# Kernel optimization log

Hardware: AMD Instinct MI355X
Metric: run time of the kernel (lower is better)

Reference implementation:

```python
import jax, jax.numpy as jnp
import numpy as np

H = 8
DK = 32
D_MODEL = H * DK


def _leaky(x):
    # LeakyReLU(negative_slope=0.1)
    return jnp.where(x > 0, x, 0.1 * x)


def _edge_feat(p_edge, W1, b1, W2, b2):
    # p_edge: [b, d_edge, n, n] -> [b, h, d_k, n, n]
    e = jnp.transpose(p_edge, (0, 2, 3, 1))          # [b, n, n, d_edge]
    e = _leaky(e @ W1 + b1) @ W2 + b2                # [b, n, n, d_model]
    b, n = e.shape[0], e.shape[1]
    e = e.reshape(b, n, n, H, DK)
    return jnp.transpose(e, (0, 3, 4, 1, 2))          # [b, h, d_k, n, n]


def setup_inputs() -> dict:
    key = jax.random.key(0)
    ks = jax.random.split(key, 24)
    b, n, d_model, d_edge, d_hidden = 2, 512, 256, 40, 32
    s = 0.05
    return {
        "query": jax.random.normal(ks[0], (b, n, d_model), jnp.float32),
        "key_": jax.random.normal(ks[1], (b, n, d_model), jnp.float32),
        "value": jax.random.normal(ks[2], (b, n, d_model), jnp.float32),
        "edges_att": jax.random.normal(ks[3], (b, d_edge, n, n), jnp.float32),
        "mask": jax.random.randint(ks[4], (b, n), 0, 2, jnp.int32),
        "Wq": jax.random.normal(ks[5], (d_model, d_model), jnp.float32) * s,
        "bq": jax.random.normal(ks[6], (d_model,), jnp.float32) * s,
        "Wk": jax.random.normal(ks[7], (d_model, d_model), jnp.float32) * s,
        "bk": jax.random.normal(ks[8], (d_model,), jnp.float32) * s,
        "Wv": jax.random.normal(ks[9], (d_model, d_model), jnp.float32) * s,
        "bv": jax.random.normal(ks[10], (d_model,), jnp.float32) * s,
        "Wo": jax.random.normal(ks[11], (d_model, d_model), jnp.float32) * s,
        "bo": jax.random.normal(ks[12], (d_model,), jnp.float32) * s,
        "rkW1": jax.random.normal(ks[13], (d_edge, d_hidden), jnp.float32) * s,
        "rkb1": jax.random.normal(ks[14], (d_hidden,), jnp.float32) * s,
        "rkW2": jax.random.normal(ks[15], (d_hidden, d_model), jnp.float32) * s,
        "rkb2": jax.random.normal(ks[16], (d_model,), jnp.float32) * s,
        "rvW1": jax.random.normal(ks[17], (d_edge, d_hidden), jnp.float32) * s,
        "rvb1": jax.random.normal(ks[18], (d_hidden,), jnp.float32) * s,
        "rvW2": jax.random.normal(ks[19], (d_hidden, d_model), jnp.float32) * s,
        "rvb2": jax.random.normal(ks[20], (d_model,), jnp.float32) * s,
        "u": jax.random.normal(ks[21], (H, DK), jnp.float32) * s,
        "v": jax.random.normal(ks[22], (H, DK), jnp.float32) * s,
    }


def reference(query, key_, value, edges_att, mask,
              Wq, bq, Wk, bk, Wv, bv, Wo, bo,
              rkW1, rkb1, rkW2, rkb2, rvW1, rvb1, rvW2, rvb2, u, v):
    b, n, _ = query.shape

    def proj(x, W, bb):
        return jnp.transpose((x @ W + bb).reshape(b, n, H, DK), (0, 2, 1, 3))  # [b,h,n,d_k]

    q = proj(query, Wq, bq)
    k = proj(key_, Wk, bk)
    val = proj(value, Wv, bv)

    relK = _edge_feat(edges_att, rkW1, rkb1, rkW2, rkb2)  # [b,h,d_k,n,n]
    relV = _edge_feat(edges_att, rvW1, rvb1, rvW2, rvb2)  # [b,h,d_k,n,n]

    inv = 1.0 / jnp.sqrt(jnp.asarray(DK, q.dtype))
    s1 = jnp.einsum('bhid,bhjd->bhij', q, k) * inv
    s2 = jnp.einsum('bhid,bhdij->bhij', q + k, relK) * inv
    s3 = jnp.einsum('bhid,hd->bhi', k, u)[..., None]      # broadcast over j
    s4 = jnp.einsum('bhdij,hd->bhij', relK, v)
    scores = s1 + s2 + s3 + s4
    scores = jnp.where(mask[:, None, None, :] == 0, jnp.asarray(-1e12, scores.dtype), scores)
    p = jax.nn.softmax(scores, axis=-1)                    # [b,h,n,n]

    o = jnp.einsum('bhij,bhjd->bhid', p, val) + jnp.einsum('bhij,bhdij->bhid', p, relV)
    x = jnp.transpose(o, (0, 2, 1, 3)).reshape(b, n, D_MODEL)
    return x @ Wo + bo
```

## Files before the change

kernel.cpp:

```cpp
#include <hip/hip_runtime.h>
#include <hip/hip_bf16.h>

#define HH 8
#define DKK 32
#define DM 256
#define NN 512
#define DE 40
#define DHID 32
#define CH 128

typedef __attribute__((ext_vector_type(4))) short short4v;
typedef __attribute__((ext_vector_type(8))) short short8v;
typedef __attribute__((ext_vector_type(4))) float f32x4;

__device__ __forceinline__ unsigned short f2bf(float x) {
    union { __hip_bfloat16 h; unsigned short u; } c;
    c.h = __float2bfloat16(x);
    return c.u;
}
__device__ __forceinline__ float bf2f(unsigned short u) {
    return __uint_as_float(((unsigned int)u) << 16);
}
__device__ __forceinline__ float bf_lo(unsigned int u){ return __uint_as_float(u << 16); }
__device__ __forceinline__ float bf_hi(unsigned int u){ return __uint_as_float(u & 0xffff0000u); }
__device__ __forceinline__ unsigned int pack2bf(float a, float b) {
    return (unsigned int)f2bf(a) | ((unsigned int)f2bf(b) << 16);
}
__device__ __forceinline__ short8v ld8(const unsigned short* p) {
    short4v lo = *(const short4v*)p;
    short4v hi = *(const short4v*)(p + 4);
    short8v r;
    r[0]=lo[0]; r[1]=lo[1]; r[2]=lo[2]; r[3]=lo[3];
    r[4]=hi[0]; r[5]=hi[1]; r[6]=hi[2]; r[7]=hi[3];
    return r;
}

__global__ __launch_bounds__(256) void proj_kernel(
    const float* __restrict__ query, const float* __restrict__ key_,
    const float* __restrict__ value,
    const float* __restrict__ Wq, const float* __restrict__ bq,
    const float* __restrict__ Wk, const float* __restrict__ bk,
    const float* __restrict__ Wv, const float* __restrict__ bv,
    float* __restrict__ Q, float* __restrict__ K, float* __restrict__ V,
    int grpPerMat)
{
    const int m  = blockIdx.x / grpPerMat;
    const int r0 = (blockIdx.x % grpPerMat) * 4;
    const float* x; const float* W; const float* bb; float* dst;
    if (m == 0)      { x = query; W = Wq; bb = bq; dst = Q; }
    else if (m == 1) { x = key_;  W = Wk; bb = bk; dst = K; }
    else             { x = value; W = Wv; bb = bv; dst = V; }
    const int c = threadIdx.x;
    const float b0 = bb[c];
    float a0 = b0, a1 = b0, a2 = b0, a3 = b0;
    for (int k = 0; k < DM; ++k) {
        const float w = W[k*DM + c];
        a0 = fmaf(x[(size_t)(r0+0)*DM + k], w, a0);
        a1 = fmaf(x[(size_t)(r0+1)*DM + k], w, a1);
        a2 = fmaf(x[(size_t)(r0+2)*DM + k], w, a2);
        a3 = fmaf(x[(size_t)(r0+3)*DM + k], w, a3);
    }
    dst[(size_t)(r0+0)*DM + c] = a0;
    dst[(size_t)(r0+1)*DM + c] = a1;
    dst[(size_t)(r0+2)*DM + c] = a2;
    dst[(size_t)(r0+3)*DM + c] = a3;
}

__global__ __launch_bounds__(256) void s1_kernel(
    const float* __restrict__ Q, const float* __restrict__ K,
    unsigned short* __restrict__ s1)
{
    const int tid = threadIdx.x;
    const int bh = blockIdx.y, b = bh >> 3, hh = bh & 7;
    const int ti = (blockIdx.x >> 3) * 64, tj = (blockIdx.x & 7) * 64;
    __shared__ float Qt[64][33];
    __shared__ float Kt[64][33];
    const int c = tid & 31, r0 = tid >> 5;
#pragma unroll
    for (int s = 0; s < 8; ++s) {
        Qt[r0 + 8*s][c] = Q[(size_t)(b*NN + ti + r0 + 8*s)*DM + hh*DKK + c];
        Kt[r0 + 8*s][c] = K[(size_t)(b*NN + tj + r0 + 8*s)*DM + hh*DKK + c];
    }
    __syncthreads();
    const int tx = tid & 15, ty = tid >> 4;
    float acc[4][4] = {};
#pragma unroll
    for (int k = 0; k < DKK; ++k) {
        float qv[4], kv[4];
#pragma unroll
        for (int u = 0; u < 4; ++u) { qv[u] = Qt[ty*4+u][k]; kv[u] = Kt[tx*4+u][k]; }
#pragma unroll
        for (int ri = 0; ri < 4; ++ri)
#pragma unroll
            for (int cj = 0; cj < 4; ++cj)
                acc[ri][cj] = fmaf(qv[ri], kv[cj], acc[ri][cj]);
    }
    const float inv = 0.17677669529663687f;
#pragma unroll
    for (int ri = 0; ri < 4; ++ri) {
        ushort4 o;
        o.x = f2bf(acc[ri][0]*inv); o.y = f2bf(acc[ri][1]*inv);
        o.z = f2bf(acc[ri][2]*inv); o.w = f2bf(acc[ri][3]*inv);
        *(ushort4*)(s1 + ((size_t)(b*HH + hh)*NN + ti + ty*4 + ri)*NN + tj + tx*4) = o;
    }
}

__global__ __launch_bounds__(256, 4) void chunk_kernel(
    const float* __restrict__ edges, const int* __restrict__ mask,
    const float* __restrict__ rkW1, const float* __restrict__ rkb1,
    const float* __restrict__ rkW2, const float* __restrict__ rkb2,
    const float* __restrict__ rvW1, const float* __restrict__ rvb1,
    const float* __restrict__ vvec,
    const float* __restrict__ Q, const float* __restrict__ K, const float* __restrict__ V,
    const unsigned short* __restrict__ s1u,
    float* __restrict__ ws_m, float* __restrict__ ws_z,
    float* __restrict__ ws_A, float* __restrict__ ws_O)
{
    const int bid = blockIdx.x;
    const int bi = bid >> 2, cq = bid & 3;
    const int b  = bi >> 9;
    const int i  = bi & 511;
    const int j0 = cq*CH;
    const int tid = threadIdx.x;
    const int h = tid >> 5, l32 = tid & 31;
    const int wid = tid >> 6, lane = tid & 63;
    const int g = lane >> 4, q16 = lane & 15;
    const int team = tid >> 6, qq = tid & 63, hq = qq >> 3;
    const int jj = tid & 127, half = tid >> 7;
    const float inv = 0.17677669529663687f;

    __shared__ __align__(16) unsigned char uni[17408];
    __shared__ __align__(16) unsigned short W1bf[64*68];
    __shared__ __align__(16) float sc[HH*132];
    __shared__ __align__(16) float gKs[HH*DKK];
    __shared__ float c0Ks[HH];

    unsigned short* E   = (unsigned short*)uni;
    unsigned short* hvT = (unsigned short*)uni;
    unsigned short* hk  = (unsigned short*)(uni + 8448);
    unsigned short* pb  = (unsigned short*)(uni + 8448);
    float* wf    = (float*)uni;
    float* paccA = (float*)uni;
    float* po    = (float*)(uni + 4096);

    const size_t ebase = (size_t)b*DE*NN*NN + (size_t)i*NN;
    const float* qrow = Q + (size_t)bi*DM;

    float ev[20];
    {
        const float* ep = edges + ebase + j0 + jj;
#pragma unroll
        for (int u = 0; u < 20; ++u) ev[u] = ep[(size_t)(half*20+u)*NN*NN];
    }

    wf[tid] = inv*(qrow[tid] + K[(size_t)bi*DM + tid]) + vvec[tid];
    {
        const int n = tid >> 2, qd = tid & 3;
#pragma unroll
        for (int kk = 0; kk < 17; ++kk) {
            const int k = qd*17 + kk;
            float v = 0.f;
            if (k < DE) v = (n < 32) ? rkW1[k*DHID + n] : rvW1[k*DHID + (n-32)];
            W1bf[n*68 + k] = f2bf(v);
        }
    }
    float biasv[4];
#pragma unroll
    for (int nt = 0; nt < 4; ++nt) {
        const int n = nt*16 + q16;
        biasv[nt] = (n < 32) ? rkb1[n] : rvb1[n-32];
    }
    __syncthreads();

    {
        float acc = 0.f;
#pragma unroll
        for (int d4 = 0; d4 < DKK/4; ++d4) {
            const float4 w4 = *(const float4*)(rkW2 + (size_t)l32*DM + h*DKK + d4*4);
            const float4 f4 = *(const float4*)(&wf[h*DKK + d4*4]);
            acc = fmaf(w4.x, f4.x, acc); acc = fmaf(w4.y, f4.y, acc);
            acc = fmaf(w4.z, f4.z, acc); acc = fmaf(w4.w, f4.w, acc);
        }
        gKs[h*DKK + l32] = acc;
        if (tid < HH) {
            float a2 = 0.f;
#pragma unroll
            for (int d = 0; d < DKK; ++d)
                a2 = fmaf(rkb2[tid*DKK + d], wf[tid*DKK + d], a2);
            c0Ks[tid] = a2;
        }
    }
    __syncthreads();

    const float* vb = V + (size_t)b*NN*DM;
    const unsigned short* s1b = s1u + (size_t)b*HH*NN*NN + (size_t)i*NN;

    {
        unsigned int* Ed = (unsigned int*)&E[jj*68 + half*20];
#pragma unroll
        for (int u = 0; u < 10; ++u) Ed[u] = pack2bf(ev[2*u], ev[2*u+1]);
        if (half) {
            unsigned int* Ez = (unsigned int*)&E[jj*68 + 40];
#pragma unroll
            for (int z = 0; z < 12; ++z) Ez[z] = 0u;
        }
    }
    __syncthreads();

    f32x4 acc[2][4];
#pragma unroll
    for (int jt = 0; jt < 2; ++jt) {
        const int jn = wid*32 + jt*16 + q16;
        short8v a0 = ld8(&E[jn*68 + g*8]);
        short8v a1 = ld8(&E[jn*68 + 32 + g*8]);
#pragma unroll
        for (int nt = 0; nt < 4; ++nt) {
            const unsigned short* wp = &W1bf[(q16 + nt*16)*68 + g*8];
            f32x4 c;
            c[0] = biasv[nt]; c[1] = biasv[nt]; c[2] = biasv[nt]; c[3] = biasv[nt];
            c = __builtin_amdgcn_mfma_f32_16x16x32_bf16(a0, ld8(wp), c, 0, 0, 0);
            c = __builtin_amdgcn_mfma_f32_16x16x32_bf16(a1, ld8(wp + 32), c, 0, 0, 0);
            acc[jt][nt] = c;
        }
    }
    __syncthreads();

#pragma unroll
    for (int jt = 0; jt < 2; ++jt) {
        const int jw = wid*32 + jt*16 + g*4;
#pragma unroll
        for (int nt = 0; nt < 4; ++nt) {
#pragma unroll
            for (int r = 0; r < 4; ++r) {
                float x = acc[jt][nt][r];
                x = x > 0.f ? x : 0.1f*x;
                const unsigned short us = f2bf(x);
                const int n = nt*16 + q16;
                if (n < 32) hk[(jw+r)*34 + n] = us;
                else        hvT[(n-32)*132 + (jw+r)] = us;
            }
        }
    }
    __syncthreads();

    {
        unsigned int hku[16];
#pragma unroll
        for (int d = 0; d < 16; ++d) hku[d] = *(const unsigned int*)&hk[jj*34 + 2*d];
        const int mk = mask[b*NN + j0 + jj];
        float racc[4];
#pragma unroll
        for (int u = 0; u < 4; ++u) racc[u] = c0Ks[half*4 + u];
#pragma unroll
        for (int d = 0; d < 16; ++d) {
            const float lo = bf_lo(hku[d]), hi = bf_hi(hku[d]);
#pragma unroll
            for (int u = 0; u < 4; ++u) {
                const int hh = half*4 + u;
                racc[u] = fmaf(gKs[hh*DKK + 2*d],     lo, racc[u]);
                racc[u] = fmaf(gKs[hh*DKK + 2*d + 1], hi, racc[u]);
            }
        }
#pragma unroll
        for (int u = 0; u < 4; ++u) {
            const int hh = half*4 + u;
            float r = racc[u] + bf2f(s1b[(size_t)hh*NN*NN + j0 + jj]);
            if (mk == 0) r = -1e12f;
            sc[hh*132 + jj] = r;
        }
    }
    __syncthreads();

    {
        float sv[4];
        float mc = -3e38f;
#pragma unroll
        for (int k = 0; k < 4; ++k) { sv[k] = sc[h*132 + l32 + 32*k]; mc = fmaxf(mc, sv[k]); }
#pragma unroll
        for (int off = 16; off; off >>= 1) mc = fmaxf(mc, __shfl_xor(mc, off, 32));
        float zc = 0.f;
#pragma unroll
        for (int k = 0; k < 4; ++k) {
            const float e = __expf(sv[k] - mc);
            pb[h*132 + l32 + 32*k] = f2bf(e);
            zc += e;
        }
#pragma unroll
        for (int off = 16; off; off >>= 1) zc += __shfl_xor(zc, off, 32);
        if (l32 == 0) {
            ws_m[(size_t)bid*8 + h] = mc;
            ws_z[(size_t)bid*8 + h] = zc;
        }
    }
    __syncthreads();

    f32x4 accAf0 = {0.f,0.f,0.f,0.f}, accAf1 = {0.f,0.f,0.f,0.f};
    float aO0 = 0.f, aO1 = 0.f, aO2 = 0.f, aO3 = 0.f;
    {
        short8v pA = ld8(&pb[q16*132 + wid*32 + g*8]);
        short8v b0 = ld8(&hvT[q16*132 + wid*32 + g*8]);
        short8v b1 = ld8(&hvT[(16+q16)*132 + wid*32 + g*8]);
        accAf0 = __builtin_amdgcn_mfma_f32_16x16x32_bf16(pA, b0, accAf0, 0, 0, 0);
        accAf1 = __builtin_amdgcn_mfma_f32_16x16x32_bf16(pA, b1, accAf1, 0, 0, 0);

        const float* vrow = vb + (size_t)(j0 + team)*DM + qq*4;
        const unsigned short* ph = pb + hq*132 + team;
#pragma unroll 4
        for (int it = 0; it < 32; ++it) {
            const float p = bf2f(ph[4*it]);
            const float4 v4 = *(const float4*)(vrow + (size_t)it*4*DM);
            aO0 = fmaf(p, v4.x, aO0); aO1 = fmaf(p, v4.y, aO1);
            aO2 = fmaf(p, v4.z, aO2); aO3 = fmaf(p, v4.w, aO3);
        }
    }
    __syncthreads();

    if (g < 2) {
#pragma unroll
        for (int r = 0; r < 4; ++r) {
            paccA[wid*256 + (4*g+r)*32 + q16]      = accAf0[r];
            paccA[wid*256 + (4*g+r)*32 + 16 + q16] = accAf1[r];
        }
    }
    *(float4*)(po + team*256 + qq*4) = make_float4(aO0, aO1, aO2, aO3);
    __syncthreads();

    ws_A[(size_t)bid*256 + tid] = paccA[tid] + paccA[256+tid] + paccA[512+tid] + paccA[768+tid];
    ws_O[(size_t)bid*256 + tid] = po[tid] + po[256+tid] + po[512+tid] + po[768+tid];
}

__global__ __launch_bounds__(256) void combine_kernel(
    const float* __restrict__ rvW2, const float* __restrict__ rvb2,
    const float* __restrict__ Wo, const float* __restrict__ bo,
    const float* __restrict__ ws_m, const float* __restrict__ ws_z,
    const float* __restrict__ ws_A, const float* __restrict__ ws_O,
    float* __restrict__ out)
{
    const int bi0 = blockIdx.x * 2;
    const int tid = threadIdx.x;
    const int h = tid >> 5;
    __shared__ float A_l[2][DM], o_l[2][DM];
    __shared__ float wqs[2][4][HH], rzs[2][HH];

    if (tid < 16) {
        const int r = tid >> 3, hh = tid & 7;
        const int bi = bi0 + r;
        float mv[4], zv[4];
#pragma unroll
        for (int q = 0; q < 4; ++q) {
            mv[q] = ws_m[(size_t)(bi*4+q)*8 + hh];
            zv[q] = ws_z[(size_t)(bi*4+q)*8 + hh];
        }
        const float mm = fmaxf(fmaxf(mv[0], mv[1]), fmaxf(mv[2], mv[3]));
        float zt = 0.f;
#pragma unroll
        for (int q = 0; q < 4; ++q) {
            const float w = __expf(mv[q] - mm);
            wqs[r][q][hh] = w;
            zt = fmaf(zv[q], w, zt);
        }
        rzs[r][hh] = 1.f / zt;
    }
    __syncthreads();

    float o1v[2];
#pragma unroll
    for (int r = 0; r < 2; ++r) {
        const int bi = bi0 + r;
        const float rz = rzs[r][h];
        float A = 0.f, o1 = 0.f;
#pragma unroll
        for (int q = 0; q < 4; ++q) {
            const float w = wqs[r][q][h];
            A  = fmaf(w, ws_A[(size_t)(bi*4+q)*256 + tid], A);
            o1 = fmaf(w, ws_O[(size_t)(bi*4+q)*256 + tid], o1);
        }
        A_l[r][tid] = A * rz;
        o1v[r] = o1 * rz;
    }
    __syncthreads();

#pragma unroll
    for (int r = 0; r < 2; ++r) {
        float o2 = rvb2[tid];
#pragma unroll
        for (int t = 0; t < DHID; ++t)
            o2 = fmaf(A_l[r][h*DKK + t], rvW2[(size_t)t*DM + tid], o2);
        o_l[r][tid] = o1v[r] + o2;
    }
    __syncthreads();

    float acc0 = bo[tid], acc1 = acc0;
#pragma unroll 4
    for (int k = 0; k < DM; ++k) {
        const float w = Wo[(size_t)k*DM + tid];
        acc0 = fmaf(o_l[0][k], w, acc0);
        acc1 = fmaf(o_l[1][k], w, acc1);
    }
    out[(size_t)(bi0+0)*DM + tid] = acc0;
    out[(size_t)(bi0+1)*DM + tid] = acc1;
}

extern "C" void kernel_launch(void* const* d_in, const int* in_sizes, int n_in,
                              void* d_out, int out_size, void* d_ws, size_t ws_size,
                              hipStream_t stream) {
    const float* query = (const float*)d_in[0];
    const float* key_  = (const float*)d_in[1];
    const float* value = (const float*)d_in[2];
    const float* edges = (const float*)d_in[3];
    const int*   mask  = (const int*)d_in[4];
    const float* Wq = (const float*)d_in[5];
    const float* bq = (const float*)d_in[6];
    const float* Wk = (const float*)d_in[7];
    const float* bk = (const float*)d_in[8];
    const float* Wv = (const float*)d_in[9];
    const float* bv = (const float*)d_in[10];
    const float* Wo = (const float*)d_in[11];
    const float* bo = (const float*)d_in[12];
    const float* rkW1 = (const float*)d_in[13];
    const float* rkb1 = (const float*)d_in[14];
    const float* rkW2 = (const float*)d_in[15];
    const float* rkb2 = (const float*)d_in[16];
    const float* rvW1 = (const float*)d_in[17];
    const float* rvb1 = (const float*)d_in[18];
    const float* rvW2 = (const float*)d_in[19];
    const float* rvb2 = (const float*)d_in[20];
    const float* vvec = (const float*)d_in[22];

    const int rows = in_sizes[0] / DM;
    const int nchunk = rows * 4;

    float* Qw = (float*)d_ws;
    float* Kw = Qw + (size_t)rows*DM;
    float* Vw = Kw + (size_t)rows*DM;
    unsigned short* s1u = (unsigned short*)(Vw + (size_t)rows*DM);
    float* ws_m = (float*)(s1u + (size_t)2*HH*NN*NN);
    float* ws_z = ws_m + (size_t)nchunk*8;
    float* ws_A = ws_z + (size_t)nchunk*8;
    float* ws_O = ws_A + (size_t)nchunk*256;

    hipLaunchKernelGGL(proj_kernel, dim3(3*rows/4), dim3(256), 0, stream,
                       query, key_, value, Wq, bq, Wk, bk, Wv, bv, Qw, Kw, Vw, rows/4);
    hipLaunchKernelGGL(s1_kernel, dim3(64, 16), dim3(256), 0, stream,
                       Qw, Kw, s1u);
    hipLaunchKernelGGL(chunk_kernel, dim3(nchunk), dim3(256), 0, stream,
                       edges, mask, rkW1, rkb1, rkW2, rkb2, rvW1, rvb1,
                       vvec, Qw, Kw, Vw, s1u, ws_m, ws_z, ws_A, ws_O);
    hipLaunchKernelGGL(combine_kernel, dim3(rows/2), dim3(256), 0, stream,
                       rvW2, rvb2, Wo, bo, ws_m, ws_z, ws_A, ws_O, (float*)d_out);
}
```

Before: 115.6 us.

## Fuse s1 into chunk kernel via MFMA and hoist per-row precompute to pre_kernel

Drops the separate s1 kernel and its bf16 score buffer in global memory. The chunk kernel now computes q·k scores directly with MFMA from bf16 Q/K copies that the projection kernel writes. The relK score term also moves to an MFMA. Per-row gK vectors and the bf16 W1 staging move into a new pre_kernel so chunk_kernel does less setup and uses less LDS, and its occupancy hint rises to 6. The cost is an extra launch, bf16 rounding of K and Q, and wasted MFMA lanes from the masked per-head B operand.

After: 117.5 us. No clear change (+1.6%).

```diff
diff --git a/kernel.cpp b/kernel.cpp
--- a/kernel.cpp
+++ b/kernel.cpp
@@ -21,8 +21,6 @@
 __device__ __forceinline__ float bf2f(unsigned short u) {
     return __uint_as_float(((unsigned int)u) << 16);
 }
-__device__ __forceinline__ float bf_lo(unsigned int u){ return __uint_as_float(u << 16); }
-__device__ __forceinline__ float bf_hi(unsigned int u){ return __uint_as_float(u & 0xffff0000u); }
 __device__ __forceinline__ unsigned int pack2bf(float a, float b) {
     return (unsigned int)f2bf(a) | ((unsigned int)f2bf(b) << 16);
 }
@@ -42,6 +40,7 @@
     const float* __restrict__ Wk, const float* __restrict__ bk,
     const float* __restrict__ Wv, const float* __restrict__ bv,
     float* __restrict__ Q, float* __restrict__ K, float* __restrict__ V,
+    unsigned short* __restrict__ qbf, unsigned short* __restrict__ Kbf,
     int grpPerMat)
 {
     const int m  = blockIdx.x / grpPerMat;
@@ -64,55 +63,73 @@
     dst[(size_t)(r0+1)*DM + c] = a1;
     dst[(size_t)(r0+2)*DM + c] = a2;
     dst[(size_t)(r0+3)*DM + c] = a3;
-}
-
-__global__ __launch_bounds__(256) void s1_kernel(
+    if (m == 0) {
+        const float inv = 0.17677669529663687f;
+        qbf[(size_t)(r0+0)*DM + c] = f2bf(a0*inv);
+        qbf[(size_t)(r0+1)*DM + c] = f2bf(a1*inv);
+        qbf[(size_t)(r0+2)*DM + c] = f2bf(a2*inv);
+        qbf[(size_t)(r0+3)*DM + c] = f2bf(a3*inv);
+    } else if (m == 1) {
+        Kbf[(size_t)(r0+0)*DM + c] = f2bf(a0);
+        Kbf[(size_t)(r0+1)*DM + c] = f2bf(a1);
+        Kbf[(size_t)(r0+2)*DM + c] = f2bf(a2);
+        Kbf[(size_t)(r0+3)*DM + c] = f2bf(a3);
+    }
+}
+
+__global__ __launch_bounds__(256) void pre_kernel(
     const float* __restrict__ Q, const float* __restrict__ K,
-    unsigned short* __restrict__ s1)
+    const float* __restrict__ vvec,
+    const float* __restrict__ rkW2, const float* __restrict__ rkb2,
+    const float* __restrict__ rkW1, const float* __restrict__ rvW1,
+    const float* __restrict__ rkb1, const float* __restrict__ rvb1,
+    float* __restrict__ gkw, unsigned short* __restrict__ w1w,
+    float* __restrict__ biasw, int rows)
 {
+    const int bid = blockIdx.x;
     const int tid = threadIdx.x;
-    const int bh = blockIdx.y, b = bh >> 3, hh = bh & 7;
-    const int ti = (blockIdx.x >> 3) * 64, tj = (blockIdx.x & 7) * 64;
-    __shared__ float Qt[64][33];
-    __shared__ float Kt[64][33];
-    const int c = tid & 31, r0 = tid >> 5;
-#pragma unroll
-    for (int s = 0; s < 8; ++s) {
-        Qt[r0 + 8*s][c] = Q[(size_t)(b*NN + ti + r0 + 8*s)*DM + hh*DKK + c];
-        Kt[r0 + 8*s][c] = K[(size_t)(b*NN + tj + r0 + 8*s)*DM + hh*DKK + c];
-    }
-    __syncthreads();
-    const int tx = tid & 15, ty = tid >> 4;
-    float acc[4][4] = {};
-#pragma unroll
-    for (int k = 0; k < DKK; ++k) {
-        float qv[4], kv[4];
-#pragma unroll
-        for (int u = 0; u < 4; ++u) { qv[u] = Qt[ty*4+u][k]; kv[u] = Kt[tx*4+u][k]; }
-#pragma unroll
-        for (int ri = 0; ri < 4; ++ri)
-#pragma unroll
-            for (int cj = 0; cj < 4; ++cj)
-                acc[ri][cj] = fmaf(qv[ri], kv[cj], acc[ri][cj]);
-    }
-    const float inv = 0.17677669529663687f;
-#pragma unroll
-    for (int ri = 0; ri < 4; ++ri) {
-        ushort4 o;
-        o.x = f2bf(acc[ri][0]*inv); o.y = f2bf(acc[ri][1]*inv);
-        o.z = f2bf(acc[ri][2]*inv); o.w = f2bf(acc[ri][3]*inv);
-        *(ushort4*)(s1 + ((size_t)(b*HH + hh)*NN + ti + ty*4 + ri)*NN + tj + tx*4) = o;
-    }
-}
-
-__global__ __launch_bounds__(256, 4) void chunk_kernel(
+    if (bid < rows) {
+        const int bi = bid;
+        const int h = tid >> 5, l32 = tid & 31;
+        const float inv = 0.17677669529663687f;
+        __shared__ __align__(16) float wf[DM];
+        wf[tid] = inv*(Q[(size_t)bi*DM + tid] + K[(size_t)bi*DM + tid]) + vvec[tid];
+        __syncthreads();
+        float acc = 0.f;
+#pragma unroll
+        for (int d4 = 0; d4 < DKK/4; ++d4) {
+            const float4 w4 = *(const float4*)(rkW2 + (size_t)l32*DM + h*DKK + d4*4);
+            const float4 f4 = *(const float4*)(&wf[h*DKK + d4*4]);
+            acc = fmaf(w4.x, f4.x, acc); acc = fmaf(w4.y, f4.y, acc);
+            acc = fmaf(w4.z, f4.z, acc); acc = fmaf(w4.w, f4.w, acc);
+        }
+        ((unsigned short*)(gkw + (size_t)bi*264))[tid] = f2bf(acc);
+        if (tid < HH) {
+            float a2 = 0.f;
+#pragma unroll
+            for (int d = 0; d < DKK; ++d)
+                a2 = fmaf(rkb2[tid*DKK + d], wf[tid*DKK + d], a2);
+            gkw[(size_t)bi*264 + 256 + tid] = a2;
+        }
+    } else {
+        const int n = tid >> 2, qd = tid & 3;
+#pragma unroll
+        for (int kk = 0; kk < 17; ++kk) {
+            const int k = qd*17 + kk;
+            float v = 0.f;
+            if (k < DE) v = (n < 32) ? rkW1[k*DHID + n] : rvW1[k*DHID + (n-32)];
+            w1w[n*68 + k] = f2bf(v);
+        }
+        if (tid < 64) biasw[tid] = (tid < 32) ? rkb1[tid] : rvb1[tid-32];
+    }
+}
+
+__global__ __launch_bounds__(256, 6) void chunk_kernel(
     const float* __restrict__ edges, const int* __restrict__ mask,
-    const float* __restrict__ rkW1, const float* __restrict__ rkb1,
-    const float* __restrict__ rkW2, const float* __restrict__ rkb2,
-    const float* __restrict__ rvW1, const float* __restrict__ rvb1,
-    const float* __restrict__ vvec,
-    const float* __restrict__ Q, const float* __restrict__ K, const float* __restrict__ V,
-    const unsigned short* __restrict__ s1u,
+    const float* __restrict__ V,
+    const unsigned short* __restrict__ qbf, const unsigned short* __restrict__ Kbf,
+    const unsigned short* __restrict__ w1w, const float* __restrict__ biasw,
+    const float* __restrict__ gkw,
     float* __restrict__ ws_m, float* __restrict__ ws_z,
     float* __restrict__ ws_A, float* __restrict__ ws_O)
 {
@@ -127,24 +144,21 @@
     const int g = lane >> 4, q16 = lane & 15;
     const int team = tid >> 6, qq = tid & 63, hq = qq >> 3;
     const int jj = tid & 127, half = tid >> 7;
-    const float inv = 0.17677669529663687f;
-
-    __shared__ __align__(16) unsigned char uni[17408];
-    __shared__ __align__(16) unsigned short W1bf[64*68];
+
+    __shared__ __align__(16) unsigned char uni[18816];
     __shared__ __align__(16) float sc[HH*132];
-    __shared__ __align__(16) float gKs[HH*DKK];
+    __shared__ __align__(16) unsigned short gkb_l[16*32];
+    __shared__ int mask_l[CH];
     __shared__ float c0Ks[HH];
 
     unsigned short* E   = (unsigned short*)uni;
     unsigned short* hvT = (unsigned short*)uni;
     unsigned short* hk  = (unsigned short*)(uni + 8448);
     unsigned short* pb  = (unsigned short*)(uni + 8448);
-    float* wf    = (float*)uni;
     float* paccA = (float*)uni;
     float* po    = (float*)(uni + 4096);
 
     const size_t ebase = (size_t)b*DE*NN*NN + (size_t)i*NN;
-    const float* qrow = Q + (size_t)bi*DM;
 
     float ev[20];
     {
@@ -153,47 +167,19 @@
         for (int u = 0; u < 20; ++u) ev[u] = ep[(size_t)(half*20+u)*NN*NN];
     }
 
-    wf[tid] = inv*(qrow[tid] + K[(size_t)bi*DM + tid]) + vvec[tid];
-    {
-        const int n = tid >> 2, qd = tid & 3;
-#pragma unroll
-        for (int kk = 0; kk < 17; ++kk) {
-            const int k = qd*17 + kk;
-            float v = 0.f;
-            if (k < DE) v = (n < 32) ? rkW1[k*DHID + n] : rvW1[k*DHID + (n-32)];
-            W1bf[n*68 + k] = f2bf(v);
-        }
-    }
+    {
+        const unsigned int* gsrc = (const unsigned int*)(gkw + (size_t)bi*264);
+        unsigned int* gdst = (unsigned int*)gkb_l;
+        gdst[tid] = (tid < 128) ? gsrc[tid] : 0u;
+        if (tid < CH) mask_l[tid] = mask[b*NN + j0 + tid];
+        if (tid < HH) c0Ks[tid] = gkw[(size_t)bi*264 + 256 + tid];
+    }
+    short8v z8 = {0,0,0,0,0,0,0,0};
+    short8v myq = z8;
+    if (q16 < HH) myq = ld8(&qbf[(size_t)bi*DM + q16*DKK + g*8]);
     float biasv[4];
 #pragma unroll
-    for (int nt = 0; nt < 4; ++nt) {
-        const int n = nt*16 + q16;
-        biasv[nt] = (n < 32) ? rkb1[n] : rvb1[n-32];
-    }
-    __syncthreads();
-
-    {
-        float acc = 0.f;
-#pragma unroll
-        for (int d4 = 0; d4 < DKK/4; ++d4) {
-            const float4 w4 = *(const float4*)(rkW2 + (size_t)l32*DM + h*DKK + d4*4);
-            const float4 f4 = *(const float4*)(&wf[h*DKK + d4*4]);
-            acc = fmaf(w4.x, f4.x, acc); acc = fmaf(w4.y, f4.y, acc);
-            acc = fmaf(w4.z, f4.z, acc); acc = fmaf(w4.w, f4.w, acc);
-        }
-        gKs[h*DKK + l32] = acc;
-        if (tid < HH) {
-            float a2 = 0.f;
-#pragma unroll
-            for (int d = 0; d < DKK; ++d)
-                a2 = fmaf(rkb2[tid*DKK + d], wf[tid*DKK + d], a2);
-            c0Ks[tid] = a2;
-        }
-    }
-    __syncthreads();
-
-    const float* vb = V + (size_t)b*NN*DM;
-    const unsigned short* s1b = s1u + (size_t)b*HH*NN*NN + (size_t)i*NN;
+    for (int nt = 0; nt < 4; ++nt) biasv[nt] = biasw[nt*16 + q16];
 
     {
         unsigned int* Ed = (unsigned int*)&E[jj*68 + half*20];
@@ -215,7 +201,7 @@
         short8v a1 = ld8(&E[jn*68 + 32 + g*8]);
 #pragma unroll
         for (int nt = 0; nt < 4; ++nt) {
-            const unsigned short* wp = &W1bf[(q16 + nt*16)*68 + g*8];
+            const unsigned short* wp = w1w + (q16 + nt*16)*68 + g*8;
             f32x4 c;
             c[0] = biasv[nt]; c[1] = biasv[nt]; c[2] = biasv[nt]; c[3] = biasv[nt];
             c = __builtin_amdgcn_mfma_f32_16x16x32_bf16(a0, ld8(wp), c, 0, 0, 0);
@@ -236,7 +222,7 @@
                 x = x > 0.f ? x : 0.1f*x;
                 const unsigned short us = f2bf(x);
                 const int n = nt*16 + q16;
-                if (n < 32) hk[(jw+r)*34 + n] = us;
+                if (n < 32) hk[(jw+r)*40 + n] = us;
                 else        hvT[(n-32)*132 + (jw+r)] = us;
             }
         }
@@ -244,29 +230,31 @@
     __syncthreads();
 
     {
-        unsigned int hku[16];
-#pragma unroll
-        for (int d = 0; d < 16; ++d) hku[d] = *(const unsigned int*)&hk[jj*34 + 2*d];
-        const int mk = mask[b*NN + j0 + jj];
-        float racc[4];
-#pragma unroll
-        for (int u = 0; u < 4; ++u) racc[u] = c0Ks[half*4 + u];
-#pragma unroll
-        for (int d = 0; d < 16; ++d) {
-            const float lo = bf_lo(hku[d]), hi = bf_hi(hku[d]);
-#pragma unroll
-            for (int u = 0; u < 4; ++u) {
-                const int hh = half*4 + u;
-                racc[u] = fmaf(gKs[hh*DKK + 2*d],     lo, racc[u]);
-                racc[u] = fmaf(gKs[hh*DKK + 2*d + 1], hi, racc[u]);
+        const unsigned short* kbase = Kbf + ((size_t)(b*NN + j0))*DM;
+        short8v gkB = ld8(&gkb_l[q16*DKK + g*8]);
+#pragma unroll
+        for (int jt = 0; jt < 2; ++jt) {
+            const int jrow = wid*32 + jt*16 + q16;
+            const float ci = (q16 < HH) ? c0Ks[q16 & 7] : 0.f;
+            f32x4 s;
+            s[0] = ci; s[1] = ci; s[2] = ci; s[3] = ci;
+#pragma unroll
+            for (int hh = 0; hh < HH; ++hh) {
+                short8v aK = ld8(&kbase[(size_t)jrow*DM + hh*DKK + g*8]);
+                short8v bq = (q16 == hh) ? myq : z8;
+                s = __builtin_amdgcn_mfma_f32_16x16x32_bf16(aK, bq, s, 0, 0, 0);
             }
-        }
-#pragma unroll
-        for (int u = 0; u < 4; ++u) {
-            const int hh = half*4 + u;
-            float r = racc[u] + bf2f(s1b[(size_t)hh*NN*NN + j0 + jj]);
-            if (mk == 0) r = -1e12f;
-            sc[hh*132 + jj] = r;
+            short8v aH = ld8(&hk[jrow*40 + g*8]);
+            s = __builtin_amdgcn_mfma_f32_16x16x32_bf16(aH, gkB, s, 0, 0, 0);
+            if (q16 < HH) {
+#pragma unroll
+                for (int r = 0; r < 4; ++r) {
+                    const int jl = wid*32 + jt*16 + g*4 + r;
+                    float v = s[r];
+                    if (mask_l[jl] == 0) v = -1e12f;
+                    sc[q16*132 + jl] = v;
+                }
+            }
         }
     }
     __syncthreads();
@@ -294,16 +282,17 @@
     }
     __syncthreads();
 
-    f32x4 accAf0 = {0.f,0.f,0.f,0.f}, accAf1 = {0.f,0.f,0.f,0.f};
-    float aO0 = 0.f, aO1 = 0.f, aO2 = 0.f, aO3 = 0.f;
+    f32x4 ca0 = {0.f,0.f,0.f,0.f}, ca1 = {0.f,0.f,0.f,0.f};
     {
         short8v pA = ld8(&pb[q16*132 + wid*32 + g*8]);
         short8v b0 = ld8(&hvT[q16*132 + wid*32 + g*8]);
         short8v b1 = ld8(&hvT[(16+q16)*132 + wid*32 + g*8]);
-        accAf0 = __builtin_amdgcn_mfma_f32_16x16x32_bf16(pA, b0, accAf0, 0, 0, 0);
-        accAf1 = __builtin_amdgcn_mfma_f32_16x16x32_bf16(pA, b1, accAf1, 0, 0, 0);
-
-        const float* vrow = vb + (size_t)(j0 + team)*DM + qq*4;
+        ca0 = __builtin_amdgcn_mfma_f32_16x16x32_bf16(pA, b0, ca0, 0, 0, 0);
+        ca1 = __builtin_amdgcn_mfma_f32_16x16x32_bf16(pA, b1, ca1, 0, 0, 0);
+    }
+    float aO0 = 0.f, aO1 = 0.f, aO2 = 0.f, aO3 = 0.f;
+    {
+        const float* vrow = V + (size_t)b*NN*DM + (size_t)(j0 + team)*DM + qq*4;
         const unsigned short* ph = pb + hq*132 + team;
 #pragma unroll 4
         for (int it = 0; it < 32; ++it) {
@@ -318,8 +307,9 @@
     if (g < 2) {
 #pragma unroll
         for (int r = 0; r < 4; ++r) {
-            paccA[wid*256 + (4*g+r)*32 + q16]      = accAf0[r];
-            paccA[wid*256 + (4*g+r)*32 + 16 + q16] = accAf1[r];
+            const int hrow = g*4 + r;
+            paccA[wid*256 + hrow*32 + q16]      = ca0[r];
+            paccA[wid*256 + hrow*32 + 16 + q16] = ca1[r];
         }
     }
     *(float4*)(po + team*256 + qq*4) = make_float4(aO0, aO1, aO2, aO3);
@@ -430,22 +420,28 @@
     const int rows = in_sizes[0] / DM;
     const int nchunk = rows * 4;
 
-    float* Qw = (float*)d_ws;
-    float* Kw = Qw + (size_t)rows*DM;
-    float* Vw = Kw + (size_t)rows*DM;
-    unsigned short* s1u = (unsigned short*)(Vw + (size_t)rows*DM);
-    float* ws_m = (float*)(s1u + (size_t)2*HH*NN*NN);
+    float* Qw   = (float*)d_ws;
+    float* Kw   = Qw + (size_t)rows*DM;
+    float* Vw   = Kw + (size_t)rows*DM;
+    float* gkw  = Vw + (size_t)rows*DM;
+    float* biasw = gkw + (size_t)rows*264;
+    float* ws_m = biasw + 64;
     float* ws_z = ws_m + (size_t)nchunk*8;
     float* ws_A = ws_z + (size_t)nchunk*8;
     float* ws_O = ws_A + (size_t)nchunk*256;
+    unsigned short* qbf = (unsigned short*)(ws_O + (size_t)nchunk*256);
+    unsigned short* Kbf = qbf + (size_t)rows*DM;
+    unsigned short* w1w = Kbf + (size_t)rows*DM;
 
     hipLaunchKernelGGL(proj_kernel, dim3(3*rows/4), dim3(256), 0, stream,
-                       query, key_, value, Wq, bq, Wk, bk, Wv, bv, Qw, Kw, Vw, rows/4);
-    hipLaunchKernelGGL(s1_kernel, dim3(64, 16), dim3(256), 0, stream,
-                       Qw, Kw, s1u);
+                       query, key_, value, Wq, bq, Wk, bk, Wv, bv,
+                       Qw, Kw, Vw, qbf, Kbf, rows/4);
+    hipLaunchKernelGGL(pre_kernel, dim3(rows + 1), dim3(256), 0, stream,
+                       Qw, Kw, vvec, rkW2, rkb2, rkW1, rvW1, rkb1, rvb1,
+                       gkw, w1w, biasw, rows);
     hipLaunchKernelGGL(chunk_kernel, dim3(nchunk), dim3(256), 0, stream,
-                       edges, mask, rkW1, rkb1, rkW2, rkb2, rvW1, rvb1,
-                       vvec, Qw, Kw, Vw, s1u, ws_m, ws_z, ws_A, ws_O);
+                       edges, mask, Vw, qbf, Kbf, w1w, biasw, gkw,
+                       ws_m, ws_z, ws_A, ws_O);
     hipLaunchKernelGGL(combine_kernel, dim3(rows/2), dim3(256), 0, stream,
                        rvW2, rvb2, Wo, bo, ws_m, ws_z, ws_A, ws_O, (float*)d_out);
 }
```
